# Performance work log

Measured on AMD Instinct MI355X. Metric: run time of the kernel, lower is better.

## Reference

```python
import jax, jax.numpy as jnp
import numpy as np

N = 100000  # nodes
E = 1600000  # edges

def gcn_layer(x, W, b, src, tgt, ew):
    # support = x @ W + b ; messages gathered at src, weighted scatter-sum into tgt
    h = x @ W + b                      # [N, F_out]
    msg = h[src] * ew[:, None]         # [E, F_out]
    return jax.ops.segment_sum(msg, tgt, num_segments=N)  # [N, F_out]

def setup_inputs() -> dict:
    key = jax.random.key(0)
    ks = jax.random.split(key, 12)
    nfeat, nhid, nclass = 256, 128, 40
    x = jax.random.normal(ks[0], (N, nfeat), dtype=jnp.float32)
    src = jax.random.randint(ks[1], (E,), 0, N)
    tgt = jax.random.randint(ks[2], (E,), 0, N)
    edge_weight = jax.random.uniform(ks[3], (E,), dtype=jnp.float32)
    def w(k, fi, fo):
        return jax.random.normal(k, (fi, fo), dtype=jnp.float32) / np.sqrt(fi)
    return {
        "x": x, "src": src, "tgt": tgt, "edge_weight": edge_weight,
        "W0": w(ks[4], nfeat, nhid), "b0": jnp.zeros((nhid,), jnp.float32),
        "W1": w(ks[5], nhid, nhid),  "b1": jnp.zeros((nhid,), jnp.float32),
        "W2": w(ks[6], nhid, nhid),  "b2": jnp.zeros((nhid,), jnp.float32),
        "W3": w(ks[7], nhid, nclass),"b3": jnp.zeros((nclass,), jnp.float32),
    }

def reference(x, src, tgt, edge_weight, W0, b0, W1, b1, W2, b2, W3, b3):
    # RESK2 with nlayers=4, eval mode (dropout = identity).
    # x0 = relu(gc0); r = x0; x1 = relu(gc1); x2 = relu(gc2) + r; out = log_softmax(gc3)
    x0 = jax.nn.relu(gcn_layer(x, W0, b0, src, tgt, edge_weight))
    r = x0
    x1 = jax.nn.relu(gcn_layer(x0, W1, b1, src, tgt, edge_weight))
    x2 = jax.nn.relu(gcn_layer(x1, W2, b2, src, tgt, edge_weight)) + r
    logits = gcn_layer(x2, W3, b3, src, tgt, edge_weight)
    return jax.nn.log_softmax(logits, axis=1)
```

## Files before the change

kernel.cpp:

```cpp
#include <hip/hip_runtime.h>
#include <hip/hip_bf16.h>


typedef __attribute__((ext_vector_type(8))) short short8;
typedef __attribute__((ext_vector_type(4))) float float4v;

#define SC_SHIFT 8
#define SC_NODES 256
#define FILL_CAP 12288
#define SRC_MASK 0x1FFFF

static __device__ __forceinline__ float bf2f_lo(unsigned int v) {
    return __uint_as_float(v << 16);
}
static __device__ __forceinline__ float bf2f_hi(unsigned int v) {
    return __uint_as_float(v & 0xffff0000u);
}
static __device__ __forceinline__ unsigned short f2bf(float f) {
    unsigned int u = __float_as_uint(f);
    u = (u + 0x7fffu + ((u >> 16) & 1u)) >> 16;
    return (unsigned short)u;
}
static __device__ __forceinline__ unsigned int packbf(float a, float b) {
    return (unsigned int)f2bf(a) | ((unsigned int)f2bf(b) << 16);
}
static __device__ __forceinline__ float pw_w(unsigned int pe) {
    return __uint_as_float((pe >> 17) << 16);
}

static __device__ __forceinline__ void acc8(float* acc, uint4 v, float wt) {
    acc[0] = fmaf(bf2f_lo(v.x), wt, acc[0]);
    acc[1] = fmaf(bf2f_hi(v.x), wt, acc[1]);
    acc[2] = fmaf(bf2f_lo(v.y), wt, acc[2]);
    acc[3] = fmaf(bf2f_hi(v.y), wt, acc[3]);
    acc[4] = fmaf(bf2f_lo(v.z), wt, acc[4]);
    acc[5] = fmaf(bf2f_hi(v.z), wt, acc[5]);
    acc[6] = fmaf(bf2f_lo(v.w), wt, acc[6]);
    acc[7] = fmaf(bf2f_hi(v.w), wt, acc[7]);
}
static __device__ __forceinline__ void acc4(float* acc, uint2 v, float wt) {
    acc[0] = fmaf(bf2f_lo(v.x), wt, acc[0]);
    acc[1] = fmaf(bf2f_hi(v.x), wt, acc[1]);
    acc[2] = fmaf(bf2f_lo(v.y), wt, acc[2]);
    acc[3] = fmaf(bf2f_hi(v.y), wt, acc[3]);
}

__global__ __launch_bounds__(256) void k_count(const int* __restrict__ tgt,
                                               int* __restrict__ chunkTot,
                                               int E, int NSC) {
    __shared__ int hist[512];
    const int tid = threadIdx.x;
    hist[tid] = 0;
    hist[tid + 256] = 0;
    __syncthreads();
#pragma unroll
    for (int r = 0; r < 4; r++) {
        int e = blockIdx.x * 4096 + r * 1024 + tid * 4;
        if (e + 3 < E) {
            int4 tv = *(const int4*)&tgt[e];
            atomicAdd(&hist[tv.x >> SC_SHIFT], 1);
            atomicAdd(&hist[tv.y >> SC_SHIFT], 1);
            atomicAdd(&hist[tv.z >> SC_SHIFT], 1);
            atomicAdd(&hist[tv.w >> SC_SHIFT], 1);
        } else {
            for (int j = 0; j < 4; j++)
                if (e + j < E) atomicAdd(&hist[tgt[e + j] >> SC_SHIFT], 1);
        }
    }
    __syncthreads();
    for (int i = tid; i < NSC; i += 256) {
        int c = hist[i];
        if (c) atomicAdd(&chunkTot[i], c);
    }
}

__global__ __launch_bounds__(512) void k_scanB(const int* __restrict__ chunkTot,
                                               int* __restrict__ chunkStart,
                                               int* __restrict__ chunkCur,
                                               int E, int NSC) {
    __shared__ int sm[512];
    const int tid = threadIdx.x;
    int v = (tid < NSC) ? chunkTot[tid] : 0;
    sm[tid] = v;
    __syncthreads();
    for (int off = 1; off < 512; off <<= 1) {
        int t = (tid >= off) ? sm[tid - off] : 0;
        __syncthreads();
        sm[tid] += t;
        __syncthreads();
    }
    int excl = sm[tid] - v;
    if (tid < NSC) {
        chunkStart[tid] = excl;
        chunkCur[tid * 32] = excl;
    }
    if (tid == 0) chunkStart[NSC] = E;
}

__global__ __launch_bounds__(512) void k_bucket(const int* __restrict__ src,
                                                const int* __restrict__ tgt,
                                                const float* __restrict__ ew,
                                                int* __restrict__ chunkCur,
                                                unsigned int* __restrict__ st_pw,
                                                unsigned char* __restrict__ st_t8,
                                                int E) {
    __shared__ int cnt[512];
    __shared__ int rk[512];
    __shared__ int bbase[512];
    const int tid = threadIdx.x;
    cnt[tid] = 0;
    rk[tid] = 0;
    __syncthreads();

    int t16[16];
    unsigned int p16[16];
#pragma unroll
    for (int r = 0; r < 4; r++) {
        int e = blockIdx.x * 8192 + r * 2048 + tid * 4;
        if (e + 3 < E) {
            int4 tv = *(const int4*)&tgt[e];
            int4 sv = *(const int4*)&src[e];
            float4 wv = *(const float4*)&ew[e];
            t16[r * 4 + 0] = tv.x; t16[r * 4 + 1] = tv.y;
            t16[r * 4 + 2] = tv.z; t16[r * 4 + 3] = tv.w;
            p16[r * 4 + 0] = ((unsigned int)f2bf(wv.x) << 17) | (unsigned int)sv.x;
            p16[r * 4 + 1] = ((unsigned int)f2bf(wv.y) << 17) | (unsigned int)sv.y;
            p16[r * 4 + 2] = ((unsigned int)f2bf(wv.z) << 17) | (unsigned int)sv.z;
            p16[r * 4 + 3] = ((unsigned int)f2bf(wv.w) << 17) | (unsigned int)sv.w;
        } else {
            for (int j = 0; j < 4; j++) {
                int ee = e + j;
                t16[r * 4 + j] = (ee < E) ? tgt[ee] : -1;
                p16[r * 4 + j] = (ee < E)
                    ? (((unsigned int)f2bf(ew[ee]) << 17) | (unsigned int)src[ee])
                    : 0u;
            }
        }
    }
#pragma unroll
    for (int j = 0; j < 16; j++)
        if (t16[j] >= 0) atomicAdd(&cnt[t16[j] >> SC_SHIFT], 1);
    __syncthreads();
    {
        int c = cnt[tid];
        bbase[tid] = c ? atomicAdd(&chunkCur[tid * 32], c) : 0;
    }
    __syncthreads();
#pragma unroll
    for (int j = 0; j < 16; j++) {
        if (t16[j] >= 0) {
            int c = t16[j] >> SC_SHIFT;
            int pos = bbase[c] + atomicAdd(&rk[c], 1);
            st_pw[pos] = p16[j];
            st_t8[pos] = (unsigned char)(t16[j] & (SC_NODES - 1));
        }
    }
}

__global__ __launch_bounds__(256) void k_fill2(const unsigned int* __restrict__ st_pw,
                                               const unsigned char* __restrict__ st_t8,
                                               const int* __restrict__ chunkStart,
                                               int* __restrict__ rowptr,
                                               unsigned int* __restrict__ perm,
                                               int N, int E, int NSC) {
    __shared__ int lhist[SC_NODES];
    __shared__ int lcur[SC_NODES];
    __shared__ unsigned int ledge[FILL_CAP];
    const int tid = threadIdx.x;
    const int b = blockIdx.x;
    const int n0 = b << SC_SHIFT;
    const int nlocal = min(SC_NODES, N - n0);
    const int sstart = chunkStart[b];
    const int send = chunkStart[b + 1];
    const int cnt = send - sstart;

    lhist[tid] = 0;
    __syncthreads();
    for (int e = sstart + tid; e < send; e += 256)
        atomicAdd(&lhist[st_t8[e]], 1);
    __syncthreads();
    int v = lhist[tid];
    __syncthreads();
    lhist[tid] = v;
    __syncthreads();
    for (int off = 1; off < 256; off <<= 1) {
        int t = (tid >= off) ? lhist[tid - off] : 0;
        __syncthreads();
        lhist[tid] += t;
        __syncthreads();
    }
    int excl = lhist[tid] - v;
    if (tid < nlocal) rowptr[n0 + tid] = sstart + excl;
    if (b == NSC - 1 && tid == 0) rowptr[N] = E;
    lcur[tid] = excl;
    __syncthreads();

    if (cnt <= FILL_CAP) {
        for (int e = sstart + tid; e < send; e += 256) {
            int lt = st_t8[e];
            int pos = atomicAdd(&lcur[lt], 1);
            ledge[pos] = st_pw[e];
        }
        __syncthreads();
        for (int i = tid; i < cnt; i += 256) perm[sstart + i] = ledge[i];
    } else {
        for (int e = sstart + tid; e < send; e += 256) {
            int lt = st_t8[e];
            int pos = atomicAdd(&lcur[lt], 1);
            perm[sstart + pos] = st_pw[e];
        }
    }
}

__global__ __launch_bounds__(256) void k_wtrans_all(
    const float* __restrict__ W0, const float* __restrict__ W1,
    const float* __restrict__ W2, const float* __restrict__ W3,
    unsigned short* __restrict__ Wt0, unsigned short* __restrict__ Wt1,
    unsigned short* __restrict__ Wt2, unsigned short* __restrict__ Wt3,
    int* __restrict__ chunkTot) {
    int idx = blockIdx.x * 256 + threadIdx.x;
    if (idx < 512) chunkTot[idx] = 0;
    if (idx < 32768) {
        int c = idx >> 8, k = idx & 255;
        Wt0[idx] = f2bf(W0[k * 128 + c]);
    } else if (idx < 49152) {
        int i = idx - 32768;
        int c = i >> 7, k = i & 127;
        Wt1[i] = f2bf(W1[k * 128 + c]);
    } else if (idx < 65536) {
        int i = idx - 49152;
        int c = i >> 7, k = i & 127;
        Wt2[i] = f2bf(W2[k * 128 + c]);
    } else if (idx < 71680) {
        int i = idx - 65536;
        int c = i >> 7, k = i & 127;
        Wt3[i] = (c < 40) ? f2bf(W3[k * 40 + c]) : 0;
    }
}

template <int K, int AF32>
__global__ __launch_bounds__(256) void k_gemm_mfma(const void* __restrict__ Av,
                                                   const unsigned short* __restrict__ Wt,
                                                   const float* __restrict__ bias,
                                                   unsigned short* __restrict__ C, int N) {
    __shared__ union {
        struct {
            unsigned short As[128 * 40];
            unsigned short Bs[128 * 40];
        } s;
        unsigned short Cs[128 * 136];
    } u;
    __shared__ float bsh[128];
    const unsigned short* A16 = (const unsigned short*)Av;
    const float* A32 = (const float*)Av;
    const int tid = threadIdx.x;
    const int wave = tid >> 6, lane = tid & 63;
    const int quad = lane >> 4, l15 = lane & 15;
    const int rowBase = blockIdx.x * 128;

    if (tid < 128) bsh[tid] = bias[tid];

    const int r0 = tid >> 1, kh = (tid & 1) * 16;
    int rg0 = rowBase + r0;
    rg0 = rg0 < N ? rg0 : N - 1;

    uint4 pa0, pa1, pb0, pb1;
    auto load_step = [&](int k0) {
        if (AF32) {
            const float* ap = &A32[(size_t)rg0 * K + k0 + kh];
            float4 f0 = *(const float4*)&ap[0];
            float4 f1 = *(const float4*)&ap[4];
            float4 f2 = *(const float4*)&ap[8];
            float4 f3 = *(const float4*)&ap[12];
            pa0.x = packbf(f0.x, f0.y); pa0.y = packbf(f0.z, f0.w);
            pa0.z = packbf(f1.x, f1.y); pa0.w = packbf(f1.z, f1.w);
            pa1.x = packbf(f2.x, f2.y); pa1.y = packbf(f2.z, f2.w);
            pa1.z = packbf(f3.x, f3.y); pa1.w = packbf(f3.z, f3.w);
        } else {
            const unsigned short* ap = &A16[(size_t)rg0 * K + k0 + kh];
            pa0 = *(const uint4*)&ap[0];
            pa1 = *(const uint4*)&ap[8];
        }
        const unsigned short* bp = &Wt[(size_t)r0 * K + k0 + kh];
        pb0 = *(const uint4*)&bp[0];
        pb1 = *(const uint4*)&bp[8];
    };

    const float4v z = {0.f, 0.f, 0.f, 0.f};
    float4v acc0[8], acc1[8];
#pragma unroll
    for (int j = 0; j < 8; j++) { acc0[j] = z; acc1[j] = z; }

    load_step(0);
    for (int k0 = 0; k0 < K; k0 += 32) {
        *(uint4*)&u.s.As[r0 * 40 + kh] = pa0;
        *(uint4*)&u.s.As[r0 * 40 + kh + 8] = pa1;
        *(uint4*)&u.s.Bs[r0 * 40 + kh] = pb0;
        *(uint4*)&u.s.Bs[r0 * 40 + kh + 8] = pb1;
        __syncthreads();
        if (k0 + 32 < K) load_step(k0 + 32);

        short8 a0 = *(const short8*)&u.s.As[(wave * 32 + l15) * 40 + quad * 8];
        short8 a1 = *(const short8*)&u.s.As[(wave * 32 + 16 + l15) * 40 + quad * 8];
#pragma unroll
        for (int c = 0; c < 8; c++) {
            short8 b = *(const short8*)&u.s.Bs[(c * 16 + l15) * 40 + quad * 8];
            acc0[c] = __builtin_amdgcn_mfma_f32_16x16x32_bf16(b, a0, acc0[c], 0, 0, 0);
            acc1[c] = __builtin_amdgcn_mfma_f32_16x16x32_bf16(b, a1, acc1[c], 0, 0, 0);
        }
        __syncthreads();
    }

#pragma unroll
    for (int c = 0; c < 8; c++) {
        int colBase = c * 16 + quad * 4;
        float4 bv = *(const float4*)&bsh[colBase];
        uint2 o0, o1;
        o0.x = packbf(acc0[c][0] + bv.x, acc0[c][1] + bv.y);
        o0.y = packbf(acc0[c][2] + bv.z, acc0[c][3] + bv.w);
        o1.x = packbf(acc1[c][0] + bv.x, acc1[c][1] + bv.y);
        o1.y = packbf(acc1[c][2] + bv.z, acc1[c][3] + bv.w);
        *(uint2*)&u.Cs[(wave * 32 + l15) * 136 + colBase] = o0;
        *(uint2*)&u.Cs[(wave * 32 + 16 + l15) * 136 + colBase] = o1;
    }
    __syncthreads();
#pragma unroll
    for (int i = 0; i < 8; i++) {
        int flat = i * 256 + tid;
        int row = flat >> 4, q = flat & 15;
        int grow = rowBase + row;
        if (grow < N) {
            uint4 v = *(const uint4*)&u.Cs[row * 136 + q * 8];
            *(uint4*)&C[(size_t)grow * 128 + q * 8] = v;
        }
    }
}

__global__ __launch_bounds__(256) void k_gemm40_mfma(const unsigned short* __restrict__ A,
                                                     const unsigned short* __restrict__ Wt3,
                                                     const float* __restrict__ bias,
                                                     unsigned short* __restrict__ C, int N) {
    __shared__ union {
        struct {
            unsigned short As[128 * 40];
            unsigned short Bs[48 * 136];
        } s;
        unsigned short Cs[128 * 40];
    } u;
    __shared__ float bsh[48];
    const int tid = threadIdx.x;
    const int wave = tid >> 6, lane = tid & 63;
    const int quad = lane >> 4, l15 = lane & 15;
    const int rowBase = blockIdx.x * 128;

    if (tid < 48) bsh[tid] = (tid < 40) ? bias[tid] : 0.f;

    const int r0 = tid >> 1, kh = (tid & 1) * 16;
    int rg0 = rowBase + r0;
    rg0 = rg0 < N ? rg0 : N - 1;

    for (int t = tid; t < 48 * 16; t += 256) {
        int r = t >> 4, kc = t & 15;
        uint4 v = *(const uint4*)&Wt3[r * 128 + kc * 8];
        *(uint4*)&u.s.Bs[r * 136 + kc * 8] = v;
    }

    uint4 pa0, pa1;
    auto load_step = [&](int k0) {
        const unsigned short* ap = &A[(size_t)rg0 * 128 + k0 + kh];
        pa0 = *(const uint4*)&ap[0];
        pa1 = *(const uint4*)&ap[8];
    };

    const float4v z = {0.f, 0.f, 0.f, 0.f};
    float4v acc0[3], acc1[3];
#pragma unroll
    for (int j = 0; j < 3; j++) { acc0[j] = z; acc1[j] = z; }

    load_step(0);
    for (int k0 = 0; k0 < 128; k0 += 32) {
        *(uint4*)&u.s.As[r0 * 40 + kh] = pa0;
        *(uint4*)&u.s.As[r0 * 40 + kh + 8] = pa1;
        __syncthreads();
        if (k0 + 32 < 128) load_step(k0 + 32);

        short8 a0 = *(const short8*)&u.s.As[(wave * 32 + l15) * 40 + quad * 8];
        short8 a1 = *(const short8*)&u.s.As[(wave * 32 + 16 + l15) * 40 + quad * 8];
#pragma unroll
        for (int c = 0; c < 3; c++) {
            short8 b = *(const short8*)&u.s.Bs[(c * 16 + l15) * 136 + k0 + quad * 8];
            acc0[c] = __builtin_amdgcn_mfma_f32_16x16x32_bf16(b, a0, acc0[c], 0, 0, 0);
            acc1[c] = __builtin_amdgcn_mfma_f32_16x16x32_bf16(b, a1, acc1[c], 0, 0, 0);
        }
        __syncthreads();
    }

#pragma unroll
    for (int c = 0; c < 3; c++) {
        int colBase = c * 16 + quad * 4;
        if (c < 2 || quad < 2) {
            float4 bv = *(const float4*)&bsh[colBase];
            uint2 o0, o1;
            o0.x = packbf(acc0[c][0] + bv.x, acc0[c][1] + bv.y);
            o0.y = packbf(acc0[c][2] + bv.z, acc0[c][3] + bv.w);
            o1.x = packbf(acc1[c][0] + bv.x, acc1[c][1] + bv.y);
            o1.y = packbf(acc1[c][2] + bv.z, acc1[c][3] + bv.w);
            *(uint2*)&u.Cs[(wave * 32 + l15) * 40 + colBase] = o0;
            *(uint2*)&u.Cs[(wave * 32 + 16 + l15) * 40 + colBase] = o1;
        }
    }
    __syncthreads();
#pragma unroll
    for (int i = 0; i < 3; i++) {
        int flat = i * 256 + tid;
        if (flat < 640) {
            int row = flat / 5, q = flat - row * 5;
            int grow = rowBase + row;
            if (grow < N) {
                uint4 v = *(const uint4*)&u.Cs[row * 40 + q * 8];
                *(uint4*)&C[(size_t)grow * 40 + q * 8] = v;
            }
        }
    }
}

__global__ __launch_bounds__(256) void k_agg128(const unsigned short* __restrict__ h,
                                                const int* __restrict__ rowptr,
                                                const unsigned int* __restrict__ perm,
                                                const unsigned short* __restrict__ resid,
                                                unsigned short* __restrict__ out, int N) {
    int node = (blockIdx.x * 256 + threadIdx.x) >> 6;
    if (node >= N) return;
    const int lane = threadIdx.x & 63;
    const int g = lane >> 4, l = lane & 15;
    const int beg = rowptr[node], end = rowptr[node + 1];
    const char* hB = (const char*)h;
    const unsigned int loff = (unsigned int)l * 16u;

    float acc[8] = {};

    int base = beg;
    for (; base + 16 <= end; base += 16) {
        unsigned int p0 = perm[base + g];
        unsigned int p1 = perm[base + g + 4];
        unsigned int p2 = perm[base + g + 8];
        unsigned int p3 = perm[base + g + 12];
        uint4 a0 = *(const uint4*)(hB + ((((p0 & SRC_MASK) << 8)) | loff));
        uint4 a1 = *(const uint4*)(hB + ((((p1 & SRC_MASK) << 8)) | loff));
        uint4 a2 = *(const uint4*)(hB + ((((p2 & SRC_MASK) << 8)) | loff));
        uint4 a3 = *(const uint4*)(hB + ((((p3 & SRC_MASK) << 8)) | loff));
        acc8(acc, a0, pw_w(p0));
        acc8(acc, a1, pw_w(p1));
        acc8(acc, a2, pw_w(p2));
        acc8(acc, a3, pw_w(p3));
    }
    const int rem = end - base;
    if (rem > 0) {
        const int last = end - 1;
        auto step = [&](int b4) {
            int e = b4 + g;
            unsigned int p = perm[e <= last ? e : last];
            uint4 a = *(const uint4*)(hB + ((((p & SRC_MASK) << 8)) | loff));
            float w = e <= last ? pw_w(p) : 0.f;
            acc8(acc, a, w);
        };
        step(base);
        if (rem > 4) step(base + 4);
        if (rem > 8) step(base + 8);
        if (rem > 12) step(base + 12);
    }

#pragma unroll
    for (int i = 0; i < 8; i++) {
        acc[i] += __shfl_xor(acc[i], 16);
        acc[i] += __shfl_xor(acc[i], 32);
    }

    if (g == 0) {
#pragma unroll
        for (int i = 0; i < 8; i++) acc[i] = fmaxf(acc[i], 0.f);
        if (resid) {
            uint4 rv = *(const uint4*)&resid[(size_t)node * 128 + l * 8];
            acc[0] += bf2f_lo(rv.x); acc[1] += bf2f_hi(rv.x);
            acc[2] += bf2f_lo(rv.y); acc[3] += bf2f_hi(rv.y);
            acc[4] += bf2f_lo(rv.z); acc[5] += bf2f_hi(rv.z);
            acc[6] += bf2f_lo(rv.w); acc[7] += bf2f_hi(rv.w);
        }
        uint4 o;
        o.x = packbf(acc[0], acc[1]);
        o.y = packbf(acc[2], acc[3]);
        o.z = packbf(acc[4], acc[5]);
        o.w = packbf(acc[6], acc[7]);
        *(uint4*)&out[(size_t)node * 128 + l * 8] = o;
    }
}

__global__ __launch_bounds__(256) void k_agg40_lsm(const unsigned short* __restrict__ h,
                                                   const int* __restrict__ rowptr,
                                                   const unsigned int* __restrict__ perm,
                                                   float* __restrict__ out, int N) {
    int node = (blockIdx.x * 256 + threadIdx.x) >> 6;
    if (node >= N) return;
    const int lane = threadIdx.x & 63;
    const int g = lane >> 4, l = lane & 15;
    const int beg = rowptr[node], end = rowptr[node + 1];
    const int lc = l < 10 ? l : 0;
    const char* hB = (const char*)h;
    const unsigned int loff = (unsigned int)lc * 8u;

    float acc[4] = {};

    int base = beg;
    for (; base + 16 <= end; base += 16) {
        unsigned int p0 = perm[base + g];
        unsigned int p1 = perm[base + g + 4];
        unsigned int p2 = perm[base + g + 8];
        unsigned int p3 = perm[base + g + 12];
        uint2 a0 = *(const uint2*)(hB + ((p0 & SRC_MASK) * 80u + loff));
        uint2 a1 = *(const uint2*)(hB + ((p1 & SRC_MASK) * 80u + loff));
        uint2 a2 = *(const uint2*)(hB + ((p2 & SRC_MASK) * 80u + loff));
        uint2 a3 = *(const uint2*)(hB + ((p3 & SRC_MASK) * 80u + loff));
        acc4(acc, a0, pw_w(p0));
        acc4(acc, a1, pw_w(p1));
        acc4(acc, a2, pw_w(p2));
        acc4(acc, a3, pw_w(p3));
    }
    const int rem = end - base;
    if (rem > 0) {
        const int last = end - 1;
        auto step = [&](int b4) {
            int e = b4 + g;
            unsigned int p = perm[e <= last ? e : last];
            uint2 a = *(const uint2*)(hB + ((p & SRC_MASK) * 80u + loff));
            float w = e <= last ? pw_w(p) : 0.f;
            acc4(acc, a, w);
        };
        step(base);
        if (rem > 4) step(base + 4);
        if (rem > 8) step(base + 8);
        if (rem > 12) step(base + 12);
    }
#pragma unroll
    for (int i = 0; i < 4; i++) {
        acc[i] += __shfl_xor(acc[i], 16);
        acc[i] += __shfl_xor(acc[i], 32);
    }

    bool vf = l < 10;
    float m = vf ? fmaxf(fmaxf(acc[0], acc[1]), fmaxf(acc[2], acc[3]))
                 : -__builtin_inff();
#pragma unroll
    for (int off = 1; off < 16; off <<= 1) m = fmaxf(m, __shfl_xor(m, off));
    float s = vf ? (expf(acc[0] - m) + expf(acc[1] - m) +
                    expf(acc[2] - m) + expf(acc[3] - m))
                 : 0.f;
#pragma unroll
    for (int off = 1; off < 16; off <<= 1) s += __shfl_xor(s, off);
    float ls = m + logf(s);
    if (g == 0 && vf) {
        float4 o = make_float4(acc[0] - ls, acc[1] - ls, acc[2] - ls, acc[3] - ls);
        *(float4*)&out[(size_t)node * 40 + l * 4] = o;
    }
}

extern "C" void kernel_launch(void* const* d_in, const int* in_sizes, int n_in,
                              void* d_out, int out_size, void* d_ws, size_t ws_size,
                              hipStream_t stream) {
    const float* x  = (const float*)d_in[0];
    const int*   src = (const int*)d_in[1];
    const int*   tgt = (const int*)d_in[2];
    const float* ew  = (const float*)d_in[3];
    const float* W0 = (const float*)d_in[4];
    const float* b0 = (const float*)d_in[5];
    const float* W1 = (const float*)d_in[6];
    const float* b1 = (const float*)d_in[7];
    const float* W2 = (const float*)d_in[8];
    const float* b2 = (const float*)d_in[9];
    const float* W3 = (const float*)d_in[10];
    const float* b3 = (const float*)d_in[11];

    const int N = in_sizes[0] / 256;
    const int E = in_sizes[1];
    const int NSC = (N + SC_NODES - 1) >> SC_SHIFT;

    char* ws = (char*)d_ws;
    size_t off = 0;
    auto alloc = [&](size_t bytes) -> void* {
        void* p = ws + off;
        off = (off + bytes + 255) & ~(size_t)255;
        return p;
    };
    unsigned short* XCb = (unsigned short*)alloc((size_t)N * 128 * 2);
    size_t hbytes = (size_t)N * 128 * 2;
    size_t sbytes = (size_t)E * 5 + 256;
    char* hbuf = (char*)alloc(hbytes > sbytes ? hbytes : sbytes);
    unsigned short* Hb = (unsigned short*)hbuf;
    unsigned int* st_pw = (unsigned int*)hbuf;
    unsigned char* st_t8 = (unsigned char*)(hbuf + (size_t)E * 4);
    char* buf1 = (char*)alloc((size_t)N * 128 * 2);
    unsigned short* XAb  = (unsigned short*)buf1;
    unsigned short* H40b = (unsigned short*)buf1;
    unsigned short* XBb  = (unsigned short*)alloc((size_t)N * 128 * 2);
    int*   rowptr    = (int*)alloc((size_t)(N + 1) * 4);
    int*   chunkTot  = (int*)alloc(512 * 4);
    int*   chunkStart= (int*)alloc(520 * 4);
    int*   chunkCur  = (int*)alloc(512 * 32 * 4);
    unsigned int* perm = (unsigned int*)alloc((size_t)E * 4);
    unsigned short* Wt0 = (unsigned short*)alloc(256 * 128 * 2);
    unsigned short* Wt1 = (unsigned short*)alloc(128 * 128 * 2);
    unsigned short* Wt2 = (unsigned short*)alloc(128 * 128 * 2);
    unsigned short* Wt3 = (unsigned short*)alloc(48 * 128 * 2);
    (void)ws_size;

    float* logits = (float*)d_out;

    k_wtrans_all<<<(71680 + 255) / 256, 256, 0, stream>>>(W0, W1, W2, W3,
                                                          Wt0, Wt1, Wt2, Wt3,
                                                          chunkTot);
    k_count<<<(E + 4095) / 4096, 256, 0, stream>>>(tgt, chunkTot, E, NSC);
    k_scanB<<<1, 512, 0, stream>>>(chunkTot, chunkStart, chunkCur, E, NSC);
    k_bucket<<<(E + 8191) / 8192, 512, 0, stream>>>(src, tgt, ew, chunkCur,
                                                    st_pw, st_t8, E);
    k_fill2<<<NSC, 256, 0, stream>>>(st_pw, st_t8, chunkStart, rowptr, perm,
                                     N, E, NSC);

    const int gGemm = (N + 127) / 128;
    const int gWave = (N + 3) / 4;

    k_gemm_mfma<256, 1><<<gGemm, 256, 0, stream>>>(x, Wt0, b0, Hb, N);
    k_agg128<<<gWave, 256, 0, stream>>>(Hb, rowptr, perm, nullptr, XAb, N);
    k_gemm_mfma<128, 0><<<gGemm, 256, 0, stream>>>(XAb, Wt1, b1, Hb, N);
    k_agg128<<<gWave, 256, 0, stream>>>(Hb, rowptr, perm, nullptr, XBb, N);
    k_gemm_mfma<128, 0><<<gGemm, 256, 0, stream>>>(XBb, Wt2, b2, Hb, N);
    k_agg128<<<gWave, 256, 0, stream>>>(Hb, rowptr, perm, XAb, XCb, N);
    k_gemm40_mfma<<<gGemm, 256, 0, stream>>>(XCb, Wt3, b3, H40b, N);
    k_agg40_lsm<<<gWave, 256, 0, stream>>>(H40b, rowptr, perm, logits, N);
}
```

Before: 513.1 us.

## Store GEMM output in feature-sliced planes and aggregate per slice

```diff
diff --git a/kernel.cpp b/kernel.cpp
--- a/kernel.cpp
+++ b/kernel.cpp
@@ -43,6 +43,9 @@
     acc[1] = fmaf(bf2f_hi(v.x), wt, acc[1]);
     acc[2] = fmaf(bf2f_lo(v.y), wt, acc[2]);
     acc[3] = fmaf(bf2f_hi(v.y), wt, acc[3]);
+}
+static __device__ __forceinline__ unsigned int addbf2(unsigned int a, unsigned int b) {
+    return packbf(bf2f_lo(a) + bf2f_lo(b), bf2f_hi(a) + bf2f_hi(b));
 }
 
 __global__ __launch_bounds__(256) void k_count(const int* __restrict__ tgt,
@@ -327,16 +330,19 @@
 #pragma unroll
     for (int i = 0; i < 8; i++) {
         int flat = i * 256 + tid;
-        int row = flat >> 4, q = flat & 15;
+        int plane = flat >> 8;
+        int r2 = flat & 255;
+        int row = r2 >> 1, half = r2 & 1;
         int grow = rowBase + row;
         if (grow < N) {
-            uint4 v = *(const uint4*)&u.Cs[row * 136 + q * 8];
-            *(uint4*)&C[(size_t)grow * 128 + q * 8] = v;
+            uint4 v = *(const uint4*)&u.Cs[row * 136 + (plane * 2 + half) * 8];
+            *(uint4*)&C[(size_t)plane * N * 16 + (size_t)grow * 16 + half * 8] = v;
         }
     }
 }
 
 __global__ __launch_bounds__(256) void k_gemm40_mfma(const unsigned short* __restrict__ A,
+                                                     const unsigned short* __restrict__ R,
                                                      const unsigned short* __restrict__ Wt3,
                                                      const float* __restrict__ bias,
                                                      unsigned short* __restrict__ C, int N) {
@@ -368,8 +374,15 @@
     uint4 pa0, pa1;
     auto load_step = [&](int k0) {
         const unsigned short* ap = &A[(size_t)rg0 * 128 + k0 + kh];
-        pa0 = *(const uint4*)&ap[0];
-        pa1 = *(const uint4*)&ap[8];
+        const unsigned short* rp = &R[(size_t)rg0 * 128 + k0 + kh];
+        uint4 xa0 = *(const uint4*)&ap[0];
+        uint4 xa1 = *(const uint4*)&ap[8];
+        uint4 xr0 = *(const uint4*)&rp[0];
+        uint4 xr1 = *(const uint4*)&rp[8];
+        pa0.x = addbf2(xa0.x, xr0.x); pa0.y = addbf2(xa0.y, xr0.y);
+        pa0.z = addbf2(xa0.z, xr0.z); pa0.w = addbf2(xa0.w, xr0.w);
+        pa1.x = addbf2(xa1.x, xr1.x); pa1.y = addbf2(xa1.y, xr1.y);
+        pa1.z = addbf2(xa1.z, xr1.z); pa1.w = addbf2(xa1.w, xr1.w);
     };
 
     const float4v z = {0.f, 0.f, 0.f, 0.f};
@@ -424,74 +437,55 @@
     }
 }
 
-__global__ __launch_bounds__(256) void k_agg128(const unsigned short* __restrict__ h,
-                                                const int* __restrict__ rowptr,
-                                                const unsigned int* __restrict__ perm,
-                                                const unsigned short* __restrict__ resid,
-                                                unsigned short* __restrict__ out, int N) {
-    int node = (blockIdx.x * 256 + threadIdx.x) >> 6;
+__global__ __launch_bounds__(256) void k_agg128s(const unsigned short* __restrict__ h,
+                                                 const int* __restrict__ rowptr,
+                                                 const unsigned int* __restrict__ perm,
+                                                 unsigned short* __restrict__ out, int N) {
+    const int slice = blockIdx.x & 7;
+    const int grp = blockIdx.x >> 3;
+    const int tid = threadIdx.x;
+    const int wave = tid >> 6, lane = tid & 63;
+    const int nd = lane >> 4;
+    const int g2 = (lane >> 1) & 7;
+    const int f = lane & 1;
+    const int node = grp * 16 + wave * 4 + nd;
     if (node >= N) return;
-    const int lane = threadIdx.x & 63;
-    const int g = lane >> 4, l = lane & 15;
+
     const int beg = rowptr[node], end = rowptr[node + 1];
-    const char* hB = (const char*)h;
-    const unsigned int loff = (unsigned int)l * 16u;
+    const char* hP = (const char*)h + (size_t)slice * N * 32;
+    const unsigned int foff = (unsigned int)f * 16u;
 
     float acc[8] = {};
 
     int base = beg;
-    for (; base + 16 <= end; base += 16) {
-        unsigned int p0 = perm[base + g];
-        unsigned int p1 = perm[base + g + 4];
-        unsigned int p2 = perm[base + g + 8];
-        unsigned int p3 = perm[base + g + 12];
-        uint4 a0 = *(const uint4*)(hB + ((((p0 & SRC_MASK) << 8)) | loff));
-        uint4 a1 = *(const uint4*)(hB + ((((p1 & SRC_MASK) << 8)) | loff));
-        uint4 a2 = *(const uint4*)(hB + ((((p2 & SRC_MASK) << 8)) | loff));
-        uint4 a3 = *(const uint4*)(hB + ((((p3 & SRC_MASK) << 8)) | loff));
-        acc8(acc, a0, pw_w(p0));
-        acc8(acc, a1, pw_w(p1));
-        acc8(acc, a2, pw_w(p2));
-        acc8(acc, a3, pw_w(p3));
-    }
-    const int rem = end - base;
-    if (rem > 0) {
+    for (; base + 8 <= end; base += 8) {
+        unsigned int p = __builtin_nontemporal_load(&perm[base + g2]);
+        uint4 a = *(const uint4*)(hP + ((p & SRC_MASK) * 32u + foff));
+        acc8(acc, a, pw_w(p));
+    }
+    if (base < end) {
         const int last = end - 1;
-        auto step = [&](int b4) {
-            int e = b4 + g;
-            unsigned int p = perm[e <= last ? e : last];
-            uint4 a = *(const uint4*)(hB + ((((p & SRC_MASK) << 8)) | loff));
-            float w = e <= last ? pw_w(p) : 0.f;
-            acc8(acc, a, w);
-        };
-        step(base);
-        if (rem > 4) step(base + 4);
-        if (rem > 8) step(base + 8);
-        if (rem > 12) step(base + 12);
+        int e = base + g2;
+        unsigned int p = __builtin_nontemporal_load(&perm[e <= last ? e : last]);
+        uint4 a = *(const uint4*)(hP + ((p & SRC_MASK) * 32u + foff));
+        float w = e <= last ? pw_w(p) : 0.f;
+        acc8(acc, a, w);
     }
 
 #pragma unroll
     for (int i = 0; i < 8; i++) {
-        acc[i] += __shfl_xor(acc[i], 16);
-        acc[i] += __shfl_xor(acc[i], 32);
-    }
-
-    if (g == 0) {
-#pragma unroll
-        for (int i = 0; i < 8; i++) acc[i] = fmaxf(acc[i], 0.f);
-        if (resid) {
-            uint4 rv = *(const uint4*)&resid[(size_t)node * 128 + l * 8];
-            acc[0] += bf2f_lo(rv.x); acc[1] += bf2f_hi(rv.x);
-            acc[2] += bf2f_lo(rv.y); acc[3] += bf2f_hi(rv.y);
-            acc[4] += bf2f_lo(rv.z); acc[5] += bf2f_hi(rv.z);
-            acc[6] += bf2f_lo(rv.w); acc[7] += bf2f_hi(rv.w);
-        }
+        acc[i] += __shfl_xor(acc[i], 2);
+        acc[i] += __shfl_xor(acc[i], 4);
+        acc[i] += __shfl_xor(acc[i], 8);
+    }
+
+    if (g2 == 0) {
         uint4 o;
-        o.x = packbf(acc[0], acc[1]);
-        o.y = packbf(acc[2], acc[3]);
-        o.z = packbf(acc[4], acc[5]);
-        o.w = packbf(acc[6], acc[7]);
-        *(uint4*)&out[(size_t)node * 128 + l * 8] = o;
+        o.x = packbf(fmaxf(acc[0], 0.f), fmaxf(acc[1], 0.f));
+        o.y = packbf(fmaxf(acc[2], 0.f), fmaxf(acc[3], 0.f));
+        o.z = packbf(fmaxf(acc[4], 0.f), fmaxf(acc[5], 0.f));
+        o.w = packbf(fmaxf(acc[6], 0.f), fmaxf(acc[7], 0.f));
+        *(uint4*)&out[(size_t)node * 128 + slice * 16 + f * 8] = o;
     }
 }
 
@@ -595,11 +589,11 @@
     size_t sbytes = (size_t)E * 5 + 256;
     char* hbuf = (char*)alloc(hbytes > sbytes ? hbytes : sbytes);
     unsigned short* Hb = (unsigned short*)hbuf;
+    unsigned short* H40b = (unsigned short*)hbuf;
     unsigned int* st_pw = (unsigned int*)hbuf;
     unsigned char* st_t8 = (unsigned char*)(hbuf + (size_t)E * 4);
     char* buf1 = (char*)alloc((size_t)N * 128 * 2);
     unsigned short* XAb  = (unsigned short*)buf1;
-    unsigned short* H40b = (unsigned short*)buf1;
     unsigned short* XBb  = (unsigned short*)alloc((size_t)N * 128 * 2);
     int*   rowptr    = (int*)alloc((size_t)(N + 1) * 4);
     int*   chunkTot  = (int*)alloc(512 * 4);
@@ -625,14 +619,15 @@
                                      N, E, NSC);
 
     const int gGemm = (N + 127) / 128;
+    const int gAgg  = ((N + 15) / 16) * 8;
     const int gWave = (N + 3) / 4;
 
     k_gemm_mfma<256, 1><<<gGemm, 256, 0, stream>>>(x, Wt0, b0, Hb, N);
-    k_agg128<<<gWave, 256, 0, stream>>>(Hb, rowptr, perm, nullptr, XAb, N);
+    k_agg128s<<<gAgg, 256, 0, stream>>>(Hb, rowptr, perm, XAb, N);
     k_gemm_mfma<128, 0><<<gGemm, 256, 0, stream>>>(XAb, Wt1, b1, Hb, N);
-    k_agg128<<<gWave, 256, 0, stream>>>(Hb, rowptr, perm, nullptr, XBb, N);
+    k_agg128s<<<gAgg, 256, 0, stream>>>(Hb, rowptr, perm, XBb, N);
     k_gemm_mfma<128, 0><<<gGemm, 256, 0, stream>>>(XBb, Wt2, b2, Hb, N);
-    k_agg128<<<gWave, 256, 0, stream>>>(Hb, rowptr, perm, XAb, XCb, N);
-    k_gemm40_mfma<<<gGemm, 256, 0, stream>>>(XCb, Wt3, b3, H40b, N);
+    k_agg128s<<<gAgg, 256, 0, stream>>>(Hb, rowptr, perm, XCb, N);
+    k_gemm40_mfma<<<gGemm, 256, 0, stream>>>(XCb, XAb, Wt3, b3, H40b, N);
     k_agg40_lsm<<<gWave, 256, 0, stream>>>(H40b, rowptr, perm, logits, N);
 }
```

New measurement: 782.8 us. 52.6% more time.

## Fuse neighbor aggregation with the following layer's GEMM in one kernel

Applied to the files above, without the earlier changes.

```diff
diff --git a/kernel.cpp b/kernel.cpp
--- a/kernel.cpp
+++ b/kernel.cpp
@@ -238,11 +238,11 @@
     }
 }
 
-template <int K, int AF32>
-__global__ __launch_bounds__(256) void k_gemm_mfma(const void* __restrict__ Av,
-                                                   const unsigned short* __restrict__ Wt,
-                                                   const float* __restrict__ bias,
-                                                   unsigned short* __restrict__ C, int N) {
+__global__ __launch_bounds__(256) void k_gemm0_mfma(const float* __restrict__ A32,
+                                                    const unsigned short* __restrict__ Wt,
+                                                    const float* __restrict__ bias,
+                                                    unsigned short* __restrict__ C, int N) {
+    const int K = 256;
     __shared__ union {
         struct {
             unsigned short As[128 * 40];
@@ -251,8 +251,6 @@
         unsigned short Cs[128 * 136];
     } u;
     __shared__ float bsh[128];
-    const unsigned short* A16 = (const unsigned short*)Av;
-    const float* A32 = (const float*)Av;
     const int tid = threadIdx.x;
     const int wave = tid >> 6, lane = tid & 63;
     const int quad = lane >> 4, l15 = lane & 15;
@@ -266,21 +264,15 @@
 
     uint4 pa0, pa1, pb0, pb1;
     auto load_step = [&](int k0) {
-        if (AF32) {
-            const float* ap = &A32[(size_t)rg0 * K + k0 + kh];
-            float4 f0 = *(const float4*)&ap[0];
-            float4 f1 = *(const float4*)&ap[4];
-            float4 f2 = *(const float4*)&ap[8];
-            float4 f3 = *(const float4*)&ap[12];
-            pa0.x = packbf(f0.x, f0.y); pa0.y = packbf(f0.z, f0.w);
-            pa0.z = packbf(f1.x, f1.y); pa0.w = packbf(f1.z, f1.w);
-            pa1.x = packbf(f2.x, f2.y); pa1.y = packbf(f2.z, f2.w);
-            pa1.z = packbf(f3.x, f3.y); pa1.w = packbf(f3.z, f3.w);
-        } else {
-            const unsigned short* ap = &A16[(size_t)rg0 * K + k0 + kh];
-            pa0 = *(const uint4*)&ap[0];
-            pa1 = *(const uint4*)&ap[8];
-        }
+        const float* ap = &A32[(size_t)rg0 * K + k0 + kh];
+        float4 f0 = *(const float4*)&ap[0];
+        float4 f1 = *(const float4*)&ap[4];
+        float4 f2 = *(const float4*)&ap[8];
+        float4 f3 = *(const float4*)&ap[12];
+        pa0.x = packbf(f0.x, f0.y); pa0.y = packbf(f0.z, f0.w);
+        pa0.z = packbf(f1.x, f1.y); pa0.w = packbf(f1.z, f1.w);
+        pa1.x = packbf(f2.x, f2.y); pa1.y = packbf(f2.z, f2.w);
+        pa1.z = packbf(f3.x, f3.y); pa1.w = packbf(f3.z, f3.w);
         const unsigned short* bp = &Wt[(size_t)r0 * K + k0 + kh];
         pb0 = *(const uint4*)&bp[0];
         pb1 = *(const uint4*)&bp[8];
@@ -336,162 +328,260 @@
     }
 }
 
-__global__ __launch_bounds__(256) void k_gemm40_mfma(const unsigned short* __restrict__ A,
-                                                     const unsigned short* __restrict__ Wt3,
-                                                     const float* __restrict__ bias,
-                                                     unsigned short* __restrict__ C, int N) {
-    __shared__ union {
-        struct {
-            unsigned short As[128 * 40];
-            unsigned short Bs[48 * 136];
-        } s;
-        unsigned short Cs[128 * 40];
-    } u;
+template <int SAVE_RESID>
+__global__ __launch_bounds__(512, 4) void k_agg_gemm(
+    const unsigned short* __restrict__ h,
+    const int* __restrict__ rowptr,
+    const unsigned int* __restrict__ perm,
+    const unsigned short* __restrict__ Wt,
+    const float* __restrict__ bias,
+    unsigned short* __restrict__ resid_out,
+    unsigned short* __restrict__ C, int N) {
+    __shared__ unsigned short As[128 * 136];
+    __shared__ unsigned short Bs[128 * 136];
+    __shared__ float bsh[128];
+    const int tid = threadIdx.x;
+    const int wave = tid >> 6, lane = tid & 63;
+    const int quad = lane >> 4, l15 = lane & 15;
+    const int g = lane >> 4, l = lane & 15;
+    const int rowBase = blockIdx.x * 128;
+
+#pragma unroll
+    for (int i = 0; i < 4; i++) {
+        int flat = i * 512 + tid;
+        int row = flat >> 4, kc = flat & 15;
+        *(uint4*)&Bs[row * 136 + kc * 8] = *(const uint4*)&Wt[row * 128 + kc * 8];
+    }
+    if (tid < 128) bsh[tid] = bias[tid];
+
+    const char* hB = (const char*)h;
+    const unsigned int loff = (unsigned int)l * 16u;
+    for (int nn = 0; nn < 16; nn++) {
+        const int nodeRow = wave * 16 + nn;
+        int node = rowBase + nodeRow;
+        const bool valid = node < N;
+        if (!valid) node = N - 1;
+        const int beg = rowptr[node], end = rowptr[node + 1];
+
+        float acc[8] = {};
+        int base = beg;
+        for (; base + 16 <= end; base += 16) {
+            unsigned int p0 = perm[base + g];
+            unsigned int p1 = perm[base + g + 4];
+            unsigned int p2 = perm[base + g + 8];
+            unsigned int p3 = perm[base + g + 12];
+            uint4 a0 = *(const uint4*)(hB + ((((p0 & SRC_MASK) << 8)) | loff));
+            uint4 a1 = *(const uint4*)(hB + ((((p1 & SRC_MASK) << 8)) | loff));
+            uint4 a2 = *(const uint4*)(hB + ((((p2 & SRC_MASK) << 8)) | loff));
+            uint4 a3 = *(const uint4*)(hB + ((((p3 & SRC_MASK) << 8)) | loff));
+            acc8(acc, a0, pw_w(p0));
+            acc8(acc, a1, pw_w(p1));
+            acc8(acc, a2, pw_w(p2));
+            acc8(acc, a3, pw_w(p3));
+        }
+        const int rem = end - base;
+        if (rem > 0) {
+            const int last = end - 1;
+            auto step = [&](int b4) {
+                int e = b4 + g;
+                unsigned int p = perm[e <= last ? e : last];
+                uint4 a = *(const uint4*)(hB + ((((p & SRC_MASK) << 8)) | loff));
+                float w = e <= last ? pw_w(p) : 0.f;
+                acc8(acc, a, w);
+            };
+            step(base);
+            if (rem > 4) step(base + 4);
+            if (rem > 8) step(base + 8);
+            if (rem > 12) step(base + 12);
+        }
+
+#pragma unroll
+        for (int i = 0; i < 8; i++) {
+            acc[i] += __shfl_xor(acc[i], 16);
+            acc[i] += __shfl_xor(acc[i], 32);
+        }
+
+        if (g == 0) {
+#pragma unroll
+            for (int i = 0; i < 8; i++) acc[i] = fmaxf(acc[i], 0.f);
+            uint4 o;
+            o.x = packbf(acc[0], acc[1]);
+            o.y = packbf(acc[2], acc[3]);
+            o.z = packbf(acc[4], acc[5]);
+            o.w = packbf(acc[6], acc[7]);
+            *(uint4*)&As[nodeRow * 136 + l * 8] = o;
+            if (SAVE_RESID && valid)
+                *(uint4*)&resid_out[(size_t)node * 128 + l * 8] = o;
+        }
+    }
+    __syncthreads();
+
+    const float4v z = {0.f, 0.f, 0.f, 0.f};
+    float4v acc0[8];
+#pragma unroll
+    for (int j = 0; j < 8; j++) acc0[j] = z;
+
+#pragma unroll
+    for (int k0 = 0; k0 < 128; k0 += 32) {
+        short8 a = *(const short8*)&As[(wave * 16 + l15) * 136 + k0 + quad * 8];
+#pragma unroll
+        for (int c = 0; c < 8; c++) {
+            short8 b = *(const short8*)&Bs[(c * 16 + l15) * 136 + k0 + quad * 8];
+            acc0[c] = __builtin_amdgcn_mfma_f32_16x16x32_bf16(b, a, acc0[c], 0, 0, 0);
+        }
+    }
+    __syncthreads();
+
+#pragma unroll
+    for (int c = 0; c < 8; c++) {
+        int colBase = c * 16 + quad * 4;
+        float4 bv = *(const float4*)&bsh[colBase];
+        uint2 o;
+        o.x = packbf(acc0[c][0] + bv.x, acc0[c][1] + bv.y);
+        o.y = packbf(acc0[c][2] + bv.z, acc0[c][3] + bv.w);
+        *(uint2*)&As[(wave * 16 + l15) * 136 + colBase] = o;
+    }
+    __syncthreads();
+#pragma unroll
+    for (int i = 0; i < 4; i++) {
+        int flat = i * 512 + tid;
+        int row = flat >> 4, q = flat & 15;
+        int grow = rowBase + row;
+        if (grow < N) {
+            uint4 v = *(const uint4*)&As[row * 136 + q * 8];
+            *(uint4*)&C[(size_t)grow * 128 + q * 8] = v;
+        }
+    }
+}
+
+__global__ __launch_bounds__(512, 4) void k_agg_gemm40(
+    const unsigned short* __restrict__ h,
+    const int* __restrict__ rowptr,
+    const unsigned int* __restrict__ perm,
+    const unsigned short* __restrict__ resid,
+    const unsigned short* __restrict__ Wt3,
+    const float* __restrict__ bias,
+    unsigned short* __restrict__ C, int N) {
+    __shared__ unsigned short As[128 * 136];
+    __shared__ unsigned short Bs[48 * 136];
     __shared__ float bsh[48];
     const int tid = threadIdx.x;
     const int wave = tid >> 6, lane = tid & 63;
     const int quad = lane >> 4, l15 = lane & 15;
+    const int g = lane >> 4, l = lane & 15;
     const int rowBase = blockIdx.x * 128;
 
+    for (int t = tid; t < 48 * 16; t += 512) {
+        int row = t >> 4, kc = t & 15;
+        *(uint4*)&Bs[row * 136 + kc * 8] = *(const uint4*)&Wt3[row * 128 + kc * 8];
+    }
     if (tid < 48) bsh[tid] = (tid < 40) ? bias[tid] : 0.f;
 
-    const int r0 = tid >> 1, kh = (tid & 1) * 16;
-    int rg0 = rowBase + r0;
-    rg0 = rg0 < N ? rg0 : N - 1;
-
-    for (int t = tid; t < 48 * 16; t += 256) {
-        int r = t >> 4, kc = t & 15;
-        uint4 v = *(const uint4*)&Wt3[r * 128 + kc * 8];
-        *(uint4*)&u.s.Bs[r * 136 + kc * 8] = v;
-    }
-
-    uint4 pa0, pa1;
-    auto load_step = [&](int k0) {
-        const unsigned short* ap = &A[(size_t)rg0 * 128 + k0 + kh];
-        pa0 = *(const uint4*)&ap[0];
-        pa1 = *(const uint4*)&ap[8];
-    };
-
-    const float4v z = {0.f, 0.f, 0.f, 0.f};
-    float4v acc0[3], acc1[3];
-#pragma unroll
-    for (int j = 0; j < 3; j++) { acc0[j] = z; acc1[j] = z; }
-
-    load_step(0);
-    for (int k0 = 0; k0 < 128; k0 += 32) {
-        *(uint4*)&u.s.As[r0 * 40 + kh] = pa0;
-        *(uint4*)&u.s.As[r0 * 40 + kh + 8] = pa1;
-        __syncthreads();
-        if (k0 + 32 < 128) load_step(k0 + 32);
-
-        short8 a0 = *(const short8*)&u.s.As[(wave * 32 + l15) * 40 + quad * 8];
-        short8 a1 = *(const short8*)&u.s.As[(wave * 32 + 16 + l15) * 40 + quad * 8];
-#pragma unroll
-        for (int c = 0; c < 3; c++) {
-            short8 b = *(const short8*)&u.s.Bs[(c * 16 + l15) * 136 + k0 + quad * 8];
-            acc0[c] = __builtin_amdgcn_mfma_f32_16x16x32_bf16(b, a0, acc0[c], 0, 0, 0);
-            acc1[c] = __builtin_amdgcn_mfma_f32_16x16x32_bf16(b, a1, acc1[c], 0, 0, 0);
-        }
-        __syncthreads();
-    }
-
-#pragma unroll
-    for (int c = 0; c < 3; c++) {
-        int colBase = c * 16 + quad * 4;
-        if (c < 2 || quad < 2) {
-            float4 bv = *(const float4*)&bsh[colBase];
-            uint2 o0, o1;
-            o0.x = packbf(acc0[c][0] + bv.x, acc0[c][1] + bv.y);
-            o0.y = packbf(acc0[c][2] + bv.z, acc0[c][3] + bv.w);
-            o1.x = packbf(acc1[c][0] + bv.x, acc1[c][1] + bv.y);
-            o1.y = packbf(acc1[c][2] + bv.z, acc1[c][3] + bv.w);
-            *(uint2*)&u.Cs[(wave * 32 + l15) * 40 + colBase] = o0;
-            *(uint2*)&u.Cs[(wave * 32 + 16 + l15) * 40 + colBase] = o1;
-        }
-    }
-    __syncthreads();
-#pragma unroll
-    for (int i = 0; i < 3; i++) {
-        int flat = i * 256 + tid;
-        if (flat < 640) {
-            int row = flat / 5, q = flat - row * 5;
-            int grow = rowBase + row;
-            if (grow < N) {
-                uint4 v = *(const uint4*)&u.Cs[row * 40 + q * 8];
-                *(uint4*)&C[(size_t)grow * 40 + q * 8] = v;
-            }
-        }
-    }
-}
-
-__global__ __launch_bounds__(256) void k_agg128(const unsigned short* __restrict__ h,
-                                                const int* __restrict__ rowptr,
-                                                const unsigned int* __restrict__ perm,
-                                                const unsigned short* __restrict__ resid,
-                                                unsigned short* __restrict__ out, int N) {
-    int node = (blockIdx.x * 256 + threadIdx.x) >> 6;
-    if (node >= N) return;
-    const int lane = threadIdx.x & 63;
-    const int g = lane >> 4, l = lane & 15;
-    const int beg = rowptr[node], end = rowptr[node + 1];
     const char* hB = (const char*)h;
     const unsigned int loff = (unsigned int)l * 16u;
-
-    float acc[8] = {};
-
-    int base = beg;
-    for (; base + 16 <= end; base += 16) {
-        unsigned int p0 = perm[base + g];
-        unsigned int p1 = perm[base + g + 4];
-        unsigned int p2 = perm[base + g + 8];
-        unsigned int p3 = perm[base + g + 12];
-        uint4 a0 = *(const uint4*)(hB + ((((p0 & SRC_MASK) << 8)) | loff));
-        uint4 a1 = *(const uint4*)(hB + ((((p1 & SRC_MASK) << 8)) | loff));
-        uint4 a2 = *(const uint4*)(hB + ((((p2 & SRC_MASK) << 8)) | loff));
-        uint4 a3 = *(const uint4*)(hB + ((((p3 & SRC_MASK) << 8)) | loff));
-        acc8(acc, a0, pw_w(p0));
-        acc8(acc, a1, pw_w(p1));
-        acc8(acc, a2, pw_w(p2));
-        acc8(acc, a3, pw_w(p3));
-    }
-    const int rem = end - base;
-    if (rem > 0) {
-        const int last = end - 1;
-        auto step = [&](int b4) {
-            int e = b4 + g;
-            unsigned int p = perm[e <= last ? e : last];
-            uint4 a = *(const uint4*)(hB + ((((p & SRC_MASK) << 8)) | loff));
-            float w = e <= last ? pw_w(p) : 0.f;
-            acc8(acc, a, w);
-        };
-        step(base);
-        if (rem > 4) step(base + 4);
-        if (rem > 8) step(base + 8);
-        if (rem > 12) step(base + 12);
-    }
-
-#pragma unroll
-    for (int i = 0; i < 8; i++) {
-        acc[i] += __shfl_xor(acc[i], 16);
-        acc[i] += __shfl_xor(acc[i], 32);
-    }
-
-    if (g == 0) {
-#pragma unroll
-        for (int i = 0; i < 8; i++) acc[i] = fmaxf(acc[i], 0.f);
-        if (resid) {
+    for (int nn = 0; nn < 16; nn++) {
+        const int nodeRow = wave * 16 + nn;
+        int node = rowBase + nodeRow;
+        const bool valid = node < N;
+        if (!valid) node = N - 1;
+        const int beg = rowptr[node], end = rowptr[node + 1];
+
+        float acc[8] = {};
+        int base = beg;
+        for (; base + 16 <= end; base += 16) {
+            unsigned int p0 = perm[base + g];
+            unsigned int p1 = perm[base + g + 4];
+            unsigned int p2 = perm[base + g + 8];
+            unsigned int p3 = perm[base + g + 12];
+            uint4 a0 = *(const uint4*)(hB + ((((p0 & SRC_MASK) << 8)) | loff));
+            uint4 a1 = *(const uint4*)(hB + ((((p1 & SRC_MASK) << 8)) | loff));
+            uint4 a2 = *(const uint4*)(hB + ((((p2 & SRC_MASK) << 8)) | loff));
+            uint4 a3 = *(const uint4*)(hB + ((((p3 & SRC_MASK) << 8)) | loff));
+            acc8(acc, a0, pw_w(p0));
+            acc8(acc, a1, pw_w(p1));
+            acc8(acc, a2, pw_w(p2));
+            acc8(acc, a3, pw_w(p3));
+        }
+        const int rem = end - base;
+        if (rem > 0) {
+            const int last = end - 1;
+            auto step = [&](int b4) {
+                int e = b4 + g;
+                unsigned int p = perm[e <= last ? e : last];
+                uint4 a = *(const uint4*)(hB + ((((p & SRC_MASK) << 8)) | loff));
+                float w = e <= last ? pw_w(p) : 0.f;
+                acc8(acc, a, w);
+            };
+            step(base);
+            if (rem > 4) step(base + 4);
+            if (rem > 8) step(base + 8);
+            if (rem > 12) step(base + 12);
+        }
+
+#pragma unroll
+        for (int i = 0; i < 8; i++) {
+            acc[i] += __shfl_xor(acc[i], 16);
+            acc[i] += __shfl_xor(acc[i], 32);
+        }
+
+        if (g == 0) {
+#pragma unroll
+            for (int i = 0; i < 8; i++) acc[i] = fmaxf(acc[i], 0.f);
             uint4 rv = *(const uint4*)&resid[(size_t)node * 128 + l * 8];
             acc[0] += bf2f_lo(rv.x); acc[1] += bf2f_hi(rv.x);
             acc[2] += bf2f_lo(rv.y); acc[3] += bf2f_hi(rv.y);
             acc[4] += bf2f_lo(rv.z); acc[5] += bf2f_hi(rv.z);
             acc[6] += bf2f_lo(rv.w); acc[7] += bf2f_hi(rv.w);
-        }
-        uint4 o;
-        o.x = packbf(acc[0], acc[1]);
-        o.y = packbf(acc[2], acc[3]);
-        o.z = packbf(acc[4], acc[5]);
-        o.w = packbf(acc[6], acc[7]);
-        *(uint4*)&out[(size_t)node * 128 + l * 8] = o;
+            uint4 o;
+            o.x = packbf(acc[0], acc[1]);
+            o.y = packbf(acc[2], acc[3]);
+            o.z = packbf(acc[4], acc[5]);
+            o.w = packbf(acc[6], acc[7]);
+            *(uint4*)&As[nodeRow * 136 + l * 8] = o;
+        }
+    }
+    __syncthreads();
+
+    const float4v z = {0.f, 0.f, 0.f, 0.f};
+    float4v acc0[3];
+#pragma unroll
+    for (int j = 0; j < 3; j++) acc0[j] = z;
+
+#pragma unroll
+    for (int k0 = 0; k0 < 128; k0 += 32) {
+        short8 a = *(const short8*)&As[(wave * 16 + l15) * 136 + k0 + quad * 8];
+#pragma unroll
+        for (int c = 0; c < 3; c++) {
+            short8 b = *(const short8*)&Bs[(c * 16 + l15) * 136 + k0 + quad * 8];
+            acc0[c] = __builtin_amdgcn_mfma_f32_16x16x32_bf16(b, a, acc0[c], 0, 0, 0);
+        }
+    }
+    __syncthreads();
+
+    unsigned short* Cs = As;
+#pragma unroll
+    for (int c = 0; c < 3; c++) {
+        int colBase = c * 16 + quad * 4;
+        if (c < 2 || quad < 2) {
+            float4 bv = *(const float4*)&bsh[colBase];
+            uint2 o;
+            o.x = packbf(acc0[c][0] + bv.x, acc0[c][1] + bv.y);
+            o.y = packbf(acc0[c][2] + bv.z, acc0[c][3] + bv.w);
+            *(uint2*)&Cs[(wave * 16 + l15) * 40 + colBase] = o;
+        }
+    }
+    __syncthreads();
+#pragma unroll
+    for (int i = 0; i < 2; i++) {
+        int flat = i * 512 + tid;
+        if (flat < 640) {
+            int row = flat / 5, q = flat - row * 5;
+            int grow = rowBase + row;
+            if (grow < N) {
+                uint4 v = *(const uint4*)&Cs[row * 40 + q * 8];
+                *(uint4*)&C[(size_t)grow * 40 + q * 8] = v;
+            }
+        }
     }
 }
 
@@ -590,7 +680,6 @@
         off = (off + bytes + 255) & ~(size_t)255;
         return p;
     };
-    unsigned short* XCb = (unsigned short*)alloc((size_t)N * 128 * 2);
     size_t hbytes = (size_t)N * 128 * 2;
     size_t sbytes = (size_t)E * 5 + 256;
     char* hbuf = (char*)alloc(hbytes > sbytes ? hbytes : sbytes);
@@ -599,8 +688,9 @@
     unsigned char* st_t8 = (unsigned char*)(hbuf + (size_t)E * 4);
     char* buf1 = (char*)alloc((size_t)N * 128 * 2);
     unsigned short* XAb  = (unsigned short*)buf1;
-    unsigned short* H40b = (unsigned short*)buf1;
-    unsigned short* XBb  = (unsigned short*)alloc((size_t)N * 128 * 2);
+    char* buf2 = (char*)alloc((size_t)N * 128 * 2);
+    unsigned short* XBb  = (unsigned short*)buf2;
+    unsigned short* H40b = (unsigned short*)buf2;
     int*   rowptr    = (int*)alloc((size_t)(N + 1) * 4);
     int*   chunkTot  = (int*)alloc(512 * 4);
     int*   chunkStart= (int*)alloc(520 * 4);
@@ -627,12 +717,9 @@
     const int gGemm = (N + 127) / 128;
     const int gWave = (N + 3) / 4;
 
-    k_gemm_mfma<256, 1><<<gGemm, 256, 0, stream>>>(x, Wt0, b0, Hb, N);
-    k_agg128<<<gWave, 256, 0, stream>>>(Hb, rowptr, perm, nullptr, XAb, N);
-    k_gemm_mfma<128, 0><<<gGemm, 256, 0, stream>>>(XAb, Wt1, b1, Hb, N);
-    k_agg128<<<gWave, 256, 0, stream>>>(Hb, rowptr, perm, nullptr, XBb, N);
-    k_gemm_mfma<128, 0><<<gGemm, 256, 0, stream>>>(XBb, Wt2, b2, Hb, N);
-    k_agg128<<<gWave, 256, 0, stream>>>(Hb, rowptr, perm, XAb, XCb, N);
-    k_gemm40_mfma<<<gGemm, 256, 0, stream>>>(XCb, Wt3, b3, H40b, N);
+    k_gemm0_mfma<<<gGemm, 256, 0, stream>>>(x, Wt0, b0, Hb, N);
+    k_agg_gemm<1><<<gGemm, 512, 0, stream>>>(Hb, rowptr, perm, Wt1, b1, XAb, XBb, N);
+    k_agg_gemm<0><<<gGemm, 512, 0, stream>>>(XBb, rowptr, perm, Wt2, b2, nullptr, Hb, N);
+    k_agg_gemm40<<<gGemm, 512, 0, stream>>>(Hb, rowptr, perm, XAb, Wt3, b3, H40b, N);
     k_agg40_lsm<<<gWave, 256, 0, stream>>>(H40b, rowptr, perm, logits, N);
 }
```

Result: slower. 597.8 us (+16.5%).
